# Optimization experiments

Hardware: AMD Instinct MI355X
Metric: run time of the kernel (lower is better)

Reference implementation:

```python
import jax, jax.numpy as jnp
import numpy as np

NUM_CHANNEL = 2                      # channels per telescope group
K = 7                                # hexagonal kernel size
N_LEV = [2048, 512, 128, 32, 8]      # pixels per level (stride-2 hex pooling ~ /4)
CHS = [2, 64, 128, 256, 512]         # channel progression n1->n_features->n2->n3->n4


def _iconv(x, idx, w, b):
    # x: [B,C,Nin], idx: [K,Nout], w: [O,C,K] -> [B,O,Nout]
    g = x[:, :, idx]                              # gather neighbours [B,C,K,Nout]
    return jnp.einsum('bckn,ock->bon', g, w) + b[None, :, None]


def _ipool(x, idx):
    # IndexedMaxPool2d: gather then max over kernel positions
    return x[:, :, idx].max(axis=2)               # [B,C,Nout]


def _bn(x, gamma, beta, eps=1e-5):
    # train-mode BatchNorm1d over (batch, pixel) dims, biased variance (torch semantics)
    m = x.mean(axis=(0, 2), keepdims=True)
    v = x.var(axis=(0, 2), keepdims=True)
    return (x - m) / jnp.sqrt(v + eps) * gamma[None, :, None] + beta[None, :, None]


def setup_inputs() -> dict:
    key = jax.random.key(0)
    ks = jax.random.split(key, 40)
    ki = iter(range(40))
    nk = lambda: ks[next(ki)]
    B = 256
    inp = {"x": jax.random.normal(nk(), (B, 2 * NUM_CHANNEL, N_LEV[0]), jnp.float32)}
    for i in range(4):
        inp[f"idx_conv{i+1}"] = jax.random.randint(nk(), (K, N_LEV[i]), 0, N_LEV[i])
        inp[f"idx_pool{i+1}"] = jax.random.randint(nk(), (K, N_LEV[i + 1]), 0, N_LEV[i])
        fan = float(CHS[i] * K)
        inp[f"w{i+1}"] = jax.random.normal(nk(), (CHS[i + 1], CHS[i], K), jnp.float32) / np.float32(np.sqrt(fan))
        inp[f"b{i+1}"] = jnp.zeros((CHS[i + 1],), jnp.float32)
        inp[f"gamma{i+1}"] = jnp.ones((CHS[i + 1],), jnp.float32)
        inp[f"beta{i+1}"] = jnp.zeros((CHS[i + 1],), jnp.float32)
    F = N_LEV[4] * CHS[4]            # 8 * 512 = 4096
    H = F // 2                       # 2048
    inp["lin1_w"] = jax.random.normal(nk(), (H, F), jnp.float32) / np.float32(np.sqrt(F))
    inp["lin1_b"] = jnp.zeros((H,), jnp.float32)
    inp["gamma5"] = jnp.ones((H,), jnp.float32)
    inp["beta5"] = jnp.zeros((H,), jnp.float32)
    inp["lin2_w"] = jax.random.normal(nk(), (3, H), jnp.float32) / np.float32(np.sqrt(H))
    inp["lin2_b"] = jnp.zeros((3,), jnp.float32)
    return inp


def reference(x, idx_conv1, idx_pool1, idx_conv2, idx_pool2, idx_conv3, idx_pool3,
              idx_conv4, idx_pool4, w1, b1, gamma1, beta1, w2, b2, gamma2, beta2,
              w3, b3, gamma3, beta3, w4, b4, gamma4, beta4,
              lin1_w, lin1_b, gamma5, beta5, lin2_w, lin2_b):
    layers = [(idx_conv1, idx_pool1, w1, b1, gamma1, beta1),
              (idx_conv2, idx_pool2, w2, b2, gamma2, beta2),
              (idx_conv3, idx_pool3, w3, b3, gamma3, beta3),
              (idx_conv4, idx_pool4, w4, b4, gamma4, beta4)]
    T = x.shape[1] // NUM_CHANNEL    # number of telescope groups (static)
    outs = []
    for i in range(T):
        o = x[:, i * NUM_CHANNEL:(i + 1) * NUM_CHANNEL, :]
        for (ic, ip, w, b, g, be) in layers:
            # conv -> pool -> bn -> relu (dropout with p=0 is identity)
            o = jax.nn.relu(_bn(_ipool(_iconv(o, ic, w, b), ip), g, be))
        outs.append(o)
    o = jnp.stack(outs, 1).mean(axis=1)          # [B, 512, 8]
    o = o.reshape(o.shape[0], -1)                # [B, 4096]
    o = o @ lin1_w.T + lin1_b                    # [B, 2048]
    m = o.mean(axis=0)
    v = o.var(axis=0)
    o = (o - m) / jnp.sqrt(v + 1e-5) * gamma5 + beta5
    o = jax.nn.relu(o)
    o = o @ lin2_w.T + lin2_b                    # [B, 3]
    cls = jax.nn.log_softmax(o[:, :2], axis=1)   # targets: class=2 (log-softmax), energy=1 (raw)
    return jnp.concatenate([cls, o[:, 2:3]], axis=1)
```

## Files before the change

### kernel.cpp

```cpp
#include <hip/hip_runtime.h>
#include <math.h>

#define B 256
#define KW 7

typedef __bf16 bf16x8 __attribute__((ext_vector_type(8)));
typedef __bf16 bf16x4 __attribute__((ext_vector_type(4)));
typedef float  f32x4  __attribute__((ext_vector_type(4)));

#define LDSW 36

__device__ __forceinline__ void block_reduce2(float& s, float& s2, float* lds) {
    for (int off = 32; off > 0; off >>= 1) {
        s  += __shfl_down(s,  off, 64);
        s2 += __shfl_down(s2, off, 64);
    }
    int wave = threadIdx.x >> 6;
    int lane = threadIdx.x & 63;
    if (lane == 0) { lds[wave * 2] = s; lds[wave * 2 + 1] = s2; }
    __syncthreads();
    if (threadIdx.x == 0) {
        s  = lds[0] + lds[2] + lds[4] + lds[6];
        s2 = lds[1] + lds[3] + lds[5] + lds[7];
    }
}

__global__ __launch_bounds__(256) void k_transpose(const float* __restrict__ x,
                                                   float* __restrict__ A0) {
    int bid = blockIdx.x;
    int nt  = bid & 63;
    int rem = bid >> 6;
    int ci  = rem & 1;
    int t   = rem >> 1;
    int n0  = nt * 32;
    __shared__ float lds[32][257];
    int tid = threadIdx.x;
    int nl  = tid & 31;
    int bq  = tid >> 5;
    int ch  = t * 2 + ci;
    for (int p = 0; p < 32; p++) {
        int b = bq + p * 8;
        lds[nl][b] = x[((size_t)b * 4 + ch) * 2048 + n0 + nl];
    }
    __syncthreads();
    for (int nl2 = 0; nl2 < 32; nl2++) {
        A0[(((size_t)t * 2048 + n0 + nl2) * 2 + ci) * B + tid] = lds[nl2][tid];
    }
}

__global__ __launch_bounds__(256) void k_convpool1(
    const float* __restrict__ act,
    float* __restrict__ P1,
    const float* __restrict__ w,
    const float* __restrict__ bias,
    const int* __restrict__ idx_conv,
    const int* __restrict__ idx_pool,
    float* __restrict__ part1c)
{
    const int Kt = 14, C_out = 64, N_in = 2048, N_out = 512;
    int bid   = blockIdx.x;
    int cot   = bid & 1;
    int colid = bid >> 1;
    int t     = colid / N_out;
    int np    = colid - t * N_out;
    int co0   = cot << 5;

    __shared__ float lds_g[14 * 256];
    __shared__ float lds_w[14 * 33];
    __shared__ int   lds_idx[KW];

    int tid = threadIdx.x;
    int cog = tid >> 6;
    int bl  = tid & 63;

    float pmax[8][4];
    #pragma unroll
    for (int i = 0; i < 8; i++)
        #pragma unroll
        for (int j = 0; j < 4; j++) pmax[i][j] = -INFINITY;

    const float* actT = act + (size_t)t * N_in * 2 * B;

    for (int kp = 0; kp < KW; kp++) {
        int nc = idx_pool[kp * N_out + np];
        if (tid < KW) lds_idx[tid] = idx_conv[tid * N_in + nc];

        float acc[8][4];
        #pragma unroll
        for (int i = 0; i < 8; i++)
            #pragma unroll
            for (int j = 0; j < 4; j++) acc[i][j] = 0.f;

        __syncthreads();
        for (int e = tid; e < 32 * Kt; e += 256) {
            int kk = e % Kt;
            int co = e / Kt;
            lds_w[kk * 33 + co] = w[(size_t)(co0 + co) * Kt + kk];
        }
        for (int r = 0; r < Kt; r++) {
            int ci  = r / KW;
            int k   = r - ci * KW;
            int col = lds_idx[k];
            lds_g[r * 256 + tid] = actT[((size_t)col * 2 + ci) * B + tid];
        }
        __syncthreads();
        for (int kk = 0; kk < Kt; kk++) {
            float g0 = lds_g[kk * 256 + bl];
            float g1 = lds_g[kk * 256 + bl + 64];
            float g2 = lds_g[kk * 256 + bl + 128];
            float g3 = lds_g[kk * 256 + bl + 192];
            const float* wr = lds_w + kk * 33 + cog * 8;
            #pragma unroll
            for (int i = 0; i < 8; i++) {
                float wv = wr[i];
                acc[i][0] = fmaf(wv, g0, acc[i][0]);
                acc[i][1] = fmaf(wv, g1, acc[i][1]);
                acc[i][2] = fmaf(wv, g2, acc[i][2]);
                acc[i][3] = fmaf(wv, g3, acc[i][3]);
            }
        }
        #pragma unroll
        for (int i = 0; i < 8; i++)
            #pragma unroll
            for (int j = 0; j < 4; j++) pmax[i][j] = fmaxf(pmax[i][j], acc[i][j]);
    }

    float* outp = P1 + (((size_t)t * N_out + np) * C_out + co0) * B;
    float* pblk = part1c + (size_t)bid * 64;
    #pragma unroll
    for (int i = 0; i < 8; i++) {
        int co = cog * 8 + i;
        float bv = bias[co0 + co];
        float s = 0.f, s2 = 0.f;
        #pragma unroll
        for (int j = 0; j < 4; j++) {
            float val = pmax[i][j] + bv;
            outp[(size_t)co * B + bl + 64 * j] = val;
            s  += val;
            s2 += val * val;
        }
        for (int o = 32; o > 0; o >>= 1) {
            s  += __shfl_down(s,  o, 64);
            s2 += __shfl_down(s2, o, 64);
        }
        if ((tid & 63) == 0) {
            pblk[co]      = s;
            pblk[32 + co] = s2;
        }
    }
}

__global__ __launch_bounds__(256) void k_finstats1(
    const float* __restrict__ part1c,
    const float* __restrict__ gamma, const float* __restrict__ beta,
    float* __restrict__ scale, float* __restrict__ shift)
{
    int idx = blockIdx.x;
    int t = idx >> 6, c = idx & 63;
    int cot = c >> 5, cl = c & 31;
    float s = 0.f, s2 = 0.f;
    for (int np = threadIdx.x; np < 512; np += 256) {
        const float* pp = part1c + (size_t)((t * 512 + np) * 2 + cot) * 64;
        s  += pp[cl];
        s2 += pp[32 + cl];
    }
    __shared__ float lds[8];
    block_reduce2(s, s2, lds);
    if (threadIdx.x == 0) {
        float cnt  = 512.f * 256.f;
        float m    = s / cnt;
        float var  = s2 / cnt - m * m;
        float istd = rsqrtf(var + 1e-5f);
        float g    = gamma[c];
        scale[idx] = istd * g;
        shift[idx] = beta[c] - m * istd * g;
    }
}

__global__ __launch_bounds__(256) void k_bnrelu1t(
    const float* __restrict__ P1,
    const float* __restrict__ sc, const float* __restrict__ sh,
    __bf16* __restrict__ act1)
{
    int bid = blockIdx.x;
    int t = bid >> 9;
    int b = threadIdx.x;
    const float* src = P1 + (size_t)bid * 64 * B;
    __bf16* dst = act1 + (size_t)bid * B * 64 + (size_t)b * 64;
    const float* scp = sc + t * 64;
    const float* shp = sh + t * 64;
    __bf16 vals[64];
    #pragma unroll
    for (int co = 0; co < 64; co++) {
        float v = src[co * B + b];
        vals[co] = (__bf16)fmaxf(fmaf(v, scp[co], shp[co]), 0.f);
    }
    #pragma unroll
    for (int j = 0; j < 8; j++)
        *(bf16x8*)(dst + j * 8) = *(bf16x8*)&vals[j * 8];
}

__global__ __launch_bounds__(256) void k_prep(
    const float* __restrict__ w2, const float* __restrict__ w3,
    const float* __restrict__ w4, const float* __restrict__ lw1,
    __bf16* __restrict__ Wr2, __bf16* __restrict__ Wr3,
    __bf16* __restrict__ Wr4, __bf16* __restrict__ w1b)
{
    const int n2 = 128 * 448, n3 = 256 * 896, n4 = 512 * 1792, n1 = (2048 * 4096) / 8;
    int idx = blockIdx.x * 256 + threadIdx.x;
    if (idx < n2) {
        int ci = idx & 63; int r = idx >> 6; int kt = r % 7; int co = r / 7;
        Wr2[idx] = (__bf16)w2[((size_t)co * 64 + ci) * 7 + kt];
        return;
    }
    idx -= n2;
    if (idx < n3) {
        int ci = idx & 127; int r = idx >> 7; int kt = r % 7; int co = r / 7;
        Wr3[idx] = (__bf16)w3[((size_t)co * 128 + ci) * 7 + kt];
        return;
    }
    idx -= n3;
    if (idx < n4) {
        int ci = idx & 255; int r = idx >> 8; int kt = r % 7; int co = r / 7;
        Wr4[idx] = (__bf16)w4[((size_t)co * 256 + ci) * 7 + kt];
        return;
    }
    idx -= n4;
    if (idx < n1) {
        const f32x4* s4 = (const f32x4*)(lw1 + (size_t)idx * 8);
        f32x4 a = s4[0], b = s4[1];
        bf16x8 v;
        v[0] = (__bf16)a[0]; v[1] = (__bf16)a[1]; v[2] = (__bf16)a[2]; v[3] = (__bf16)a[3];
        v[4] = (__bf16)b[0]; v[5] = (__bf16)b[1]; v[6] = (__bf16)b[2]; v[7] = (__bf16)b[3];
        *(bf16x8*)(w1b + (size_t)idx * 8) = v;
    }
}

__global__ __launch_bounds__(256) void k_conv_mfma(
    const __bf16* __restrict__ act,
    __bf16* __restrict__ convo,
    const __bf16* __restrict__ wr,
    const int* __restrict__ idx_conv,
    int C_in, int C_out, int N, int ci_shift)
{
    int nco = C_out >> 7;
    int bid = blockIdx.x;
    int cot = bid % nco;
    int rem = bid / nco;
    int n   = rem % N;
    int t   = rem / N;
    int co0 = cot * 128;
    int Kt  = C_in * KW;

    __shared__ __bf16 lds_w[128 * LDSW];

    int tid  = threadIdx.x;
    int wv   = tid >> 6;
    int lane = tid & 63;
    int quad = lane >> 4;
    int lid  = lane & 15;

    int cols[KW];
    #pragma unroll
    for (int k = 0; k < KW; k++) cols[k] = idx_conv[k * N + n];

    f32x4 acc[8][4];
    #pragma unroll
    for (int i = 0; i < 8; i++)
        #pragma unroll
        for (int j = 0; j < 4; j++) {
            acc[i][j][0] = 0.f; acc[i][j][1] = 0.f;
            acc[i][j][2] = 0.f; acc[i][j][3] = 0.f;
        }

    const __bf16* actT = act + (size_t)t * N * B * C_in
                             + ((size_t)(wv * 64 + lid)) * C_in + quad * 8;
    int wco = tid >> 1;
    int wh  = tid & 1;
    const __bf16* wsrc = wr + (size_t)(co0 + wco) * Kt + wh * 16;

    int niter = Kt >> 5;

    bf16x8 bcur[4], bnxt[4];
    {
        const __bf16* g = actT + (size_t)cols[0] * B * C_in;
        #pragma unroll
        for (int bt = 0; bt < 4; bt++)
            bcur[bt] = *(const bf16x8*)(g + (size_t)bt * 16 * C_in);
    }

    for (int it = 0; it < niter; it++) {
        int k0 = it << 5;
        __syncthreads();
        *(bf16x8*)&lds_w[wco * LDSW + wh * 16]     = *(const bf16x8*)(wsrc + k0);
        *(bf16x8*)&lds_w[wco * LDSW + wh * 16 + 8] = *(const bf16x8*)(wsrc + k0 + 8);
        __syncthreads();
        if (it + 1 < niter) {
            int k1  = k0 + 32;
            int kt  = k1 >> ci_shift;
            int ci0 = k1 & (C_in - 1);
            const __bf16* g = actT + (size_t)cols[kt] * B * C_in + ci0;
            #pragma unroll
            for (int bt = 0; bt < 4; bt++)
                bnxt[bt] = *(const bf16x8*)(g + (size_t)bt * 16 * C_in);
        }
        #pragma unroll
        for (int rt = 0; rt < 8; rt++) {
            bf16x8 afrag = *(const bf16x8*)&lds_w[(rt * 16 + lid) * LDSW + quad * 8];
            #pragma unroll
            for (int bt = 0; bt < 4; bt++)
                acc[rt][bt] = __builtin_amdgcn_mfma_f32_16x16x32_bf16(
                    afrag, bcur[bt], acc[rt][bt], 0, 0, 0);
        }
        #pragma unroll
        for (int bt = 0; bt < 4; bt++) bcur[bt] = bnxt[bt];
    }

    __bf16* outp = convo + ((size_t)(t * N + n) * B) * C_out;
    #pragma unroll
    for (int rt = 0; rt < 8; rt++)
        #pragma unroll
        for (int bt = 0; bt < 4; bt++) {
            int b  = wv * 64 + bt * 16 + lid;
            int co = co0 + rt * 16 + quad * 4;
            bf16x4 v;
            v[0] = (__bf16)acc[rt][bt][0];
            v[1] = (__bf16)acc[rt][bt][1];
            v[2] = (__bf16)acc[rt][bt][2];
            v[3] = (__bf16)acc[rt][bt][3];
            *(bf16x4*)(outp + (size_t)b * C_out + co) = v;
        }
}

__global__ __launch_bounds__(256) void k_poolstats(
    const __bf16* __restrict__ convo,
    float* __restrict__ P,
    const float* __restrict__ bias,
    const int* __restrict__ idx_pool,
    float* __restrict__ part,
    int C, int N, int No)
{
    int bid  = blockIdx.x;
    int bg   = bid & 3;
    int rem  = bid >> 2;
    int np   = rem % No;
    int t    = rem / No;
    int cols[7];
    #pragma unroll
    for (int k = 0; k < 7; k++) cols[k] = idx_pool[k * No + np];
    const __bf16* base = convo + (size_t)t * N * B * C;
    float* pout = P + ((size_t)(t * No + np) * B) * C;
    int tid = threadIdx.x;
    float s[2] = {0.f, 0.f}, s2[2] = {0.f, 0.f};
    int NC, c0, bstart, bstep, nb;
    if (C >= 256) { NC = C >> 8; c0 = tid;           bstart = 0;        bstep = 1; nb = 64; }
    else          { NC = 1;      c0 = tid & (C - 1); bstart = tid >> 7; bstep = 2; nb = 32; }
    for (int j = 0; j < NC; j++) {
        int c = c0 + j * 256;
        float bv = bias[c];
        for (int i = 0; i < nb; i++) {
            int b = bg * 64 + bstart + i * bstep;
            float m = -1e30f;
            #pragma unroll
            for (int k = 0; k < 7; k++) {
                float v = (float)base[((size_t)cols[k] * B + b) * C + c];
                m = fmaxf(m, v);
            }
            float val = m + bv;
            pout[(size_t)b * C + c] = val;
            s[j] += val; s2[j] += val * val;
        }
    }
    float* pp = part + (size_t)((t * No + np) * 4 + bg) * 1024;
    for (int j = 0; j < NC; j++) {
        pp[tid + j * 256]       = s[j];
        pp[512 + tid + j * 256] = s2[j];
    }
}

__global__ __launch_bounds__(256) void k_finstats(
    const float* __restrict__ part,
    const float* __restrict__ gamma, const float* __restrict__ beta,
    float* __restrict__ scale, float* __restrict__ shift,
    int C, int No)
{
    int idx = blockIdx.x;
    int t = idx / C, c = idx - t * C;
    int SMAX   = C < 256 ? 256 : C;
    int nslice = SMAX / C;
    int nblk   = No * 4;
    int total  = nblk * nslice;
    const float* pbase = part + (size_t)(t * No * 4) * 1024;
    float s = 0.f, s2 = 0.f;
    for (int e = threadIdx.x; e < total; e += 256) {
        int blk = e / nslice;
        int j   = e - blk * nslice;
        const float* pp = pbase + (size_t)blk * 1024;
        int sl = c + j * C;
        s  += pp[sl];
        s2 += pp[512 + sl];
    }
    __shared__ float lds[8];
    block_reduce2(s, s2, lds);
    if (threadIdx.x == 0) {
        float cnt  = (float)No * 256.f;
        float m    = s / cnt;
        float var  = s2 / cnt - m * m;
        float istd = rsqrtf(var + 1e-5f);
        float g    = gamma[c];
        scale[idx] = istd * g;
        shift[idx] = beta[c] - m * istd * g;
    }
}

__global__ void k_bnrelu(const float* __restrict__ P, __bf16* __restrict__ act,
                         const float* __restrict__ scale, const float* __restrict__ shift,
                         int C, int total)
{
    int idx = blockIdx.x * 256 + threadIdx.x;
    if (idx >= total) return;
    int c = idx & (C - 1);
    int t = idx >= (total >> 1) ? 1 : 0;
    int tc = t * C + c;
    float v = P[idx];
    act[idx] = (__bf16)fmaxf(fmaf(v, scale[tc], shift[tc]), 0.f);
}

__global__ __launch_bounds__(256) void k_zbuild(const float* __restrict__ P4,
                                                const float* __restrict__ sc4,
                                                const float* __restrict__ sh4,
                                                __bf16* __restrict__ z)
{
    int b = blockIdx.x;
    int tid = threadIdx.x;
    for (int j = 0; j < 2; j++) {
        int c = tid + j * 256;
        float s0 = sc4[c],       h0 = sh4[c];
        float s1 = sc4[512 + c], h1 = sh4[512 + c];
        #pragma unroll
        for (int np = 0; np < 8; np++) {
            float v0 = P4[(((size_t)0 * 8 + np) * B + b) * 512 + c];
            float v1 = P4[(((size_t)1 * 8 + np) * B + b) * 512 + c];
            float y0 = fmaxf(fmaf(v0, s0, h0), 0.f);
            float y1 = fmaxf(fmaf(v1, s1, h1), 0.f);
            z[(size_t)b * 4096 + c * 8 + np] = (__bf16)(0.5f * (y0 + y1));
        }
    }
}

__global__ __launch_bounds__(256) void k_lin1_part(
    const __bf16* __restrict__ zb,
    const __bf16* __restrict__ w1b,
    float* __restrict__ partL)
{
    int ht = blockIdx.x >> 3;
    int ks = blockIdx.x & 7;
    int h0 = ht * 64;
    int f_beg = ks * 512, f_end = f_beg + 512;

    int tid  = threadIdx.x;
    int wv   = tid >> 6;
    int lane = tid & 63;
    int quad = lane >> 4;
    int lid  = lane & 15;

    f32x4 acc[4][4];
    #pragma unroll
    for (int i = 0; i < 4; i++)
        #pragma unroll
        for (int j = 0; j < 4; j++) {
            acc[i][j][0] = 0.f; acc[i][j][1] = 0.f;
            acc[i][j][2] = 0.f; acc[i][j][3] = 0.f;
        }

    const __bf16* wbase = w1b + (size_t)(h0 + lid) * 4096 + quad * 8;
    const __bf16* zbase = zb + ((size_t)(wv * 64 + lid)) * 4096 + quad * 8;

    for (int f0 = f_beg; f0 < f_end; f0 += 32) {
        bf16x8 afrag[4];
        #pragma unroll
        for (int rt = 0; rt < 4; rt++)
            afrag[rt] = *(const bf16x8*)(wbase + (size_t)rt * 16 * 4096 + f0);
        bf16x8 bfrag[4];
        #pragma unroll
        for (int bt = 0; bt < 4; bt++)
            bfrag[bt] = *(const bf16x8*)(zbase + (size_t)bt * 16 * 4096 + f0);
        #pragma unroll
        for (int rt = 0; rt < 4; rt++)
            #pragma unroll
            for (int bt = 0; bt < 4; bt++)
                acc[rt][bt] = __builtin_amdgcn_mfma_f32_16x16x32_bf16(
                    afrag[rt], bfrag[bt], acc[rt][bt], 0, 0, 0);
    }
    float* outp = partL + (size_t)ks * 2048 * B;
    #pragma unroll
    for (int rt = 0; rt < 4; rt++)
        #pragma unroll
        for (int bt = 0; bt < 4; bt++) {
            int b = wv * 64 + bt * 16 + lid;
            int h = h0 + rt * 16 + quad * 4;
            #pragma unroll
            for (int r = 0; r < 4; r++)
                outp[(size_t)(h + r) * B + b] = acc[rt][bt][r];
        }
}

__global__ __launch_bounds__(256) void k_redstats5(
    const float* __restrict__ partL,
    const float* __restrict__ b1,
    const float* __restrict__ gamma5, const float* __restrict__ beta5,
    float* __restrict__ o1,
    float* __restrict__ scale5, float* __restrict__ shift5)
{
    int h = blockIdx.x;
    int b = threadIdx.x;
    float v = b1[h];
    #pragma unroll
    for (int s = 0; s < 8; s++)
        v += partL[((size_t)s * 2048 + h) * B + b];
    o1[(size_t)h * B + b] = v;
    float s1 = v, s2 = v * v;
    __shared__ float lds[8];
    block_reduce2(s1, s2, lds);
    if (threadIdx.x == 0) {
        float m    = s1 * (1.f / 256.f);
        float var  = s2 * (1.f / 256.f) - m * m;
        float istd = rsqrtf(var + 1e-5f);
        float g    = gamma5[h];
        scale5[h]  = istd * g;
        shift5[h]  = beta5[h] - m * istd * g;
    }
}

__global__ __launch_bounds__(256) void k_final(
    const float* __restrict__ o1,
    const float* __restrict__ scale5, const float* __restrict__ shift5,
    const float* __restrict__ w2, const float* __restrict__ b2,
    float* __restrict__ out)
{
    int b = blockIdx.x;
    int tid = threadIdx.x;
    float s0 = 0.f, s1 = 0.f, s2v = 0.f;
    for (int h = tid; h < 2048; h += 256) {
        float y = fmaxf(fmaf(o1[(size_t)h * B + b], scale5[h], shift5[h]), 0.f);
        s0  = fmaf(y, w2[h],        s0);
        s1  = fmaf(y, w2[2048 + h], s1);
        s2v = fmaf(y, w2[4096 + h], s2v);
    }
    for (int off = 32; off > 0; off >>= 1) {
        s0  += __shfl_down(s0,  off, 64);
        s1  += __shfl_down(s1,  off, 64);
        s2v += __shfl_down(s2v, off, 64);
    }
    __shared__ float lds[12];
    int wave = tid >> 6, lane = tid & 63;
    if (lane == 0) { lds[wave * 3] = s0; lds[wave * 3 + 1] = s1; lds[wave * 3 + 2] = s2v; }
    __syncthreads();
    if (tid == 0) {
        float o0 = lds[0] + lds[3] + lds[6] + lds[9]  + b2[0];
        float oa = lds[1] + lds[4] + lds[7] + lds[10] + b2[1];
        float ob = lds[2] + lds[5] + lds[8] + lds[11] + b2[2];
        float m   = fmaxf(o0, oa);
        float lse = m + logf(expf(o0 - m) + expf(oa - m));
        out[b * 3 + 0] = o0 - lse;
        out[b * 3 + 1] = oa - lse;
        out[b * 3 + 2] = ob;
    }
}

extern "C" void kernel_launch(void* const* d_in, const int* in_sizes, int n_in,
                              void* d_out, int out_size, void* d_ws, size_t ws_size,
                              hipStream_t stream) {
    (void)in_sizes; (void)n_in; (void)out_size; (void)ws_size;

    const float* x   = (const float*)d_in[0];
    const int*   ic1 = (const int*)d_in[1];
    const int*   ip1 = (const int*)d_in[2];
    const float* pW1 = (const float*)d_in[3];
    const float* pB1 = (const float*)d_in[4];
    const float* pG1 = (const float*)d_in[5];
    const float* pE1 = (const float*)d_in[6];
    const int*   ic2 = (const int*)d_in[7];
    const int*   ip2 = (const int*)d_in[8];
    const float* pW2 = (const float*)d_in[9];
    const float* pB2 = (const float*)d_in[10];
    const float* pG2 = (const float*)d_in[11];
    const float* pE2 = (const float*)d_in[12];
    const int*   ic3 = (const int*)d_in[13];
    const int*   ip3 = (const int*)d_in[14];
    const float* pW3 = (const float*)d_in[15];
    const float* pB3 = (const float*)d_in[16];
    const float* pG3 = (const float*)d_in[17];
    const float* pE3 = (const float*)d_in[18];
    const int*   ic4 = (const int*)d_in[19];
    const int*   ip4 = (const int*)d_in[20];
    const float* pW4 = (const float*)d_in[21];
    const float* pB4 = (const float*)d_in[22];
    const float* pG4 = (const float*)d_in[23];
    const float* pE4 = (const float*)d_in[24];
    const float* lw1 = (const float*)d_in[25];
    const float* lb1 = (const float*)d_in[26];
    const float* g5  = (const float*)d_in[27];
    const float* e5  = (const float*)d_in[28];
    const float* lw2 = (const float*)d_in[29];
    const float* lb2 = (const float*)d_in[30];

    char* ws = (char*)d_ws;
    size_t off = 0;
    auto alloc = [&](size_t bytes) -> char* {
        char* p = ws + off;
        off += (bytes + 511) & ~(size_t)511;
        return p;
    };

    float*  A0    = (float*) alloc((size_t)2 * 2048 * 2 * B * 4);
    __bf16* act1  = (__bf16*)alloc((size_t)2 * 512 * B * 64 * 2);
    char*   U     =          alloc((size_t)512 * B * 128 * 4);
    float*  P1f   = (float*)U;
    __bf16* convX = (__bf16*)U;
    float*  partL = (float*)U;
    float*  Pf    = (float*) alloc((size_t)2 * 128 * B * 128 * 4);
    __bf16* actS  = (__bf16*)alloc((size_t)2 * 128 * B * 128 * 2);
    __bf16* Wr2   = (__bf16*)alloc((size_t)128 * 448 * 2);
    __bf16* Wr3   = (__bf16*)alloc((size_t)256 * 896 * 2);
    __bf16* Wr4   = (__bf16*)alloc((size_t)512 * 1792 * 2);
    __bf16* w1b   = (__bf16*)alloc((size_t)2048 * 4096 * 2);
    __bf16* z     = (__bf16*)alloc((size_t)256 * 4096 * 2);
    float*  o1    = (float*) alloc((size_t)2048 * B * 4);
    float*  part  = (float*) alloc((size_t)2 * 128 * 4 * 1024 * 4);
    float*  part1c= (float*) alloc((size_t)2048 * 64 * 4);
    float*  sc1 = (float*)alloc(2 * 64 * 4);
    float*  sh1 = (float*)alloc(2 * 64 * 4);
    float*  sc2 = (float*)alloc(2 * 128 * 4);
    float*  sh2 = (float*)alloc(2 * 128 * 4);
    float*  sc3 = (float*)alloc(2 * 256 * 4);
    float*  sh3 = (float*)alloc(2 * 256 * 4);
    float*  sc4 = (float*)alloc(2 * 512 * 4);
    float*  sh4 = (float*)alloc(2 * 512 * 4);
    float*  sc5 = (float*)alloc(2048 * 4);
    float*  sh5 = (float*)alloc(2048 * 4);

    {
        const int total = 128 * 448 + 256 * 896 + 512 * 1792 + (2048 * 4096) / 8;
        k_prep<<<(total + 255) / 256, 256, 0, stream>>>(pW2, pW3, pW4, lw1,
                                                        Wr2, Wr3, Wr4, w1b);
    }

    k_transpose<<<256, 256, 0, stream>>>(x, A0);

    k_convpool1<<<2048, 256, 0, stream>>>(A0, P1f, pW1, pB1, ic1, ip1, part1c);
    k_finstats1<<<2 * 64, 256, 0, stream>>>(part1c, pG1, pE1, sc1, sh1);
    k_bnrelu1t<<<2 * 512, 256, 0, stream>>>(P1f, sc1, sh1, act1);

    k_conv_mfma<<<1 * 512 * 2, 256, 0, stream>>>(act1, convX, Wr2, ic2, 64, 128, 512, 6);
    k_poolstats<<<2 * 128 * 4, 256, 0, stream>>>(convX, Pf, pB2, ip2, part, 128, 512, 128);
    k_finstats<<<2 * 128, 256, 0, stream>>>(part, pG2, pE2, sc2, sh2, 128, 128);
    k_bnrelu<<<(2 * 128 * B * 128) / 256, 256, 0, stream>>>(Pf, actS, sc2, sh2, 128, 2 * 128 * B * 128);

    k_conv_mfma<<<2 * 128 * 2, 256, 0, stream>>>(actS, convX, Wr3, ic3, 128, 256, 128, 7);
    k_poolstats<<<2 * 32 * 4, 256, 0, stream>>>(convX, Pf, pB3, ip3, part, 256, 128, 32);
    k_finstats<<<2 * 256, 256, 0, stream>>>(part, pG3, pE3, sc3, sh3, 256, 32);
    k_bnrelu<<<(2 * 32 * B * 256) / 256, 256, 0, stream>>>(Pf, actS, sc3, sh3, 256, 2 * 32 * B * 256);

    k_conv_mfma<<<4 * 32 * 2, 256, 0, stream>>>(actS, convX, Wr4, ic4, 256, 512, 32, 8);
    k_poolstats<<<2 * 8 * 4, 256, 0, stream>>>(convX, Pf, pB4, ip4, part, 512, 32, 8);
    k_finstats<<<2 * 512, 256, 0, stream>>>(part, pG4, pE4, sc4, sh4, 512, 8);

    k_zbuild<<<256, 256, 0, stream>>>(Pf, sc4, sh4, z);
    k_lin1_part<<<256, 256, 0, stream>>>(z, w1b, partL);
    k_redstats5<<<2048, 256, 0, stream>>>(partL, lb1, g5, e5, o1, sc5, sh5);
    k_final<<<256, 256, 0, stream>>>(o1, sc5, sh5, lw2, lb2, (float*)d_out);
}
```

Before: 615.2 us.

## Double-buffer conv weight tiles in LDS and prefetch activations two steps ahead

The MFMA conv kernel now keeps two LDS weight buffers. The next weight tile is loaded into registers before the MFMAs and written to the other buffer afterward, so each iteration needs one barrier instead of two. The activation gather is prefetched two iterations ahead to hide global-load latency. This costs double the LDS for weights and extra vector registers for the prefetch buffers, which may reduce occupancy.

```diff
diff --git a/kernel.cpp b/kernel.cpp
--- a/kernel.cpp
+++ b/kernel.cpp
@@ -252,7 +252,7 @@
     int co0 = cot * 128;
     int Kt  = C_in * KW;
 
-    __shared__ __bf16 lds_w[128 * LDSW];
+    __shared__ __bf16 lds_w[2][128 * LDSW];
 
     int tid  = threadIdx.x;
     int wv   = tid >> 6;
@@ -281,39 +281,61 @@
 
     int niter = Kt >> 5;
 
-    bf16x8 bcur[4], bnxt[4];
+    bf16x8 bcur[4], bn1[4], bn2[4];
+    bf16x8 wreg0, wreg1;
+
     {
-        const __bf16* g = actT + (size_t)cols[0] * B * C_in;
+        const __bf16* g0 = actT + (size_t)cols[0] * B * C_in;
         #pragma unroll
         for (int bt = 0; bt < 4; bt++)
-            bcur[bt] = *(const bf16x8*)(g + (size_t)bt * 16 * C_in);
+            bcur[bt] = *(const bf16x8*)(g0 + (size_t)bt * 16 * C_in);
+        if (niter > 1) {
+            int k1 = 32;
+            int kt = k1 >> ci_shift;
+            int ci0 = k1 & (C_in - 1);
+            const __bf16* g1 = actT + (size_t)cols[kt] * B * C_in + ci0;
+            #pragma unroll
+            for (int bt = 0; bt < 4; bt++)
+                bn1[bt] = *(const bf16x8*)(g1 + (size_t)bt * 16 * C_in);
+        }
+        wreg0 = *(const bf16x8*)(wsrc);
+        wreg1 = *(const bf16x8*)(wsrc + 8);
+        *(bf16x8*)&lds_w[0][wco * LDSW + wh * 16]     = wreg0;
+        *(bf16x8*)&lds_w[0][wco * LDSW + wh * 16 + 8] = wreg1;
+        __syncthreads();
     }
 
     for (int it = 0; it < niter; it++) {
-        int k0 = it << 5;
-        __syncthreads();
-        *(bf16x8*)&lds_w[wco * LDSW + wh * 16]     = *(const bf16x8*)(wsrc + k0);
-        *(bf16x8*)&lds_w[wco * LDSW + wh * 16 + 8] = *(const bf16x8*)(wsrc + k0 + 8);
-        __syncthreads();
+        int cur = it & 1;
         if (it + 1 < niter) {
-            int k1  = k0 + 32;
-            int kt  = k1 >> ci_shift;
-            int ci0 = k1 & (C_in - 1);
+            int k1 = (it + 1) << 5;
+            wreg0 = *(const bf16x8*)(wsrc + k1);
+            wreg1 = *(const bf16x8*)(wsrc + k1 + 8);
+        }
+        if (it + 2 < niter) {
+            int k2  = (it + 2) << 5;
+            int kt  = k2 >> ci_shift;
+            int ci0 = k2 & (C_in - 1);
             const __bf16* g = actT + (size_t)cols[kt] * B * C_in + ci0;
             #pragma unroll
             for (int bt = 0; bt < 4; bt++)
-                bnxt[bt] = *(const bf16x8*)(g + (size_t)bt * 16 * C_in);
+                bn2[bt] = *(const bf16x8*)(g + (size_t)bt * 16 * C_in);
         }
         #pragma unroll
         for (int rt = 0; rt < 8; rt++) {
-            bf16x8 afrag = *(const bf16x8*)&lds_w[(rt * 16 + lid) * LDSW + quad * 8];
+            bf16x8 afrag = *(const bf16x8*)&lds_w[cur][(rt * 16 + lid) * LDSW + quad * 8];
             #pragma unroll
             for (int bt = 0; bt < 4; bt++)
                 acc[rt][bt] = __builtin_amdgcn_mfma_f32_16x16x32_bf16(
                     afrag, bcur[bt], acc[rt][bt], 0, 0, 0);
         }
-        #pragma unroll
-        for (int bt = 0; bt < 4; bt++) bcur[bt] = bnxt[bt];
+        if (it + 1 < niter) {
+            *(bf16x8*)&lds_w[1 - cur][wco * LDSW + wh * 16]     = wreg0;
+            *(bf16x8*)&lds_w[1 - cur][wco * LDSW + wh * 16 + 8] = wreg1;
+            __syncthreads();
+        }
+        #pragma unroll
+        for (int bt = 0; bt < 4; bt++) { bcur[bt] = bn1[bt]; bn1[bt] = bn2[bt]; }
     }
 
     __bf16* outp = convo + ((size_t)(t * N + n) * B) * C_out;
```

After: 641.8 us. +4.3%, slower.
